# Kernel optimization log

Hardware: AMD Instinct MI355X
Metric: run time of the kernel (lower is better)

Reference implementation:

```python
import jax, jax.numpy as jnp
import numpy as np

NODE_DIM = 128
CAT = 16
N_NODES = 100000
N_EDGES = 200000
N_SCALARS = 6
INPUT_DIM = 5 * NODE_DIM + 5 * CAT + N_SCALARS  # 726
CELL_H, NET_H, OUT = 192, 128, 128
EPS = 1e-5


def setup_inputs() -> dict:
    key = jax.random.key(0)
    ks = jax.random.split(key, 24)
    inp = {
        'h_nodes': jax.random.normal(ks[0], (N_NODES, NODE_DIM), jnp.float32),
        'edge_scalars': jax.random.normal(ks[1], (N_EDGES, N_SCALARS), jnp.float32),
        'edge_src': jax.random.randint(ks[2], (N_EDGES,), 0, N_NODES),
        'edge_dst': jax.random.randint(ks[3], (N_EDGES,), 0, N_NODES),
        'edge_type': jax.random.randint(ks[4], (N_EDGES,), 0, 2),
        'cell_type_src': jax.random.randint(ks[5], (N_EDGES,), 0, 256),
        'cell_type_dst': jax.random.randint(ks[6], (N_EDGES,), 0, 256),
        'pin_role_src': jax.random.randint(ks[7], (N_EDGES,), 0, 64),
        'pin_role_dst': jax.random.randint(ks[8], (N_EDGES,), 0, 64),
        # embedding tables
        'emb_edge_type': jax.random.normal(ks[9], (2, CAT), jnp.float32),
        'emb_cell_type': jax.random.normal(ks[10], (256, CAT), jnp.float32),
        'emb_pin_role': jax.random.normal(ks[11], (64, CAT), jnp.float32),
        # cell MLP params
        'cell_W1': jax.random.normal(ks[12], (INPUT_DIM, CELL_H), jnp.float32) * (1.0 / np.sqrt(INPUT_DIM)),
        'cell_b1': jnp.zeros((CELL_H,), jnp.float32),
        'cell_g': jnp.ones((CELL_H,), jnp.float32),
        'cell_beta': jnp.zeros((CELL_H,), jnp.float32),
        'cell_W2': jax.random.normal(ks[13], (CELL_H, OUT), jnp.float32) * (1.0 / np.sqrt(CELL_H)),
        'cell_b2': jnp.zeros((OUT,), jnp.float32),
        # net MLP params
        'net_W1': jax.random.normal(ks[14], (INPUT_DIM, NET_H), jnp.float32) * (1.0 / np.sqrt(INPUT_DIM)),
        'net_b1': jnp.zeros((NET_H,), jnp.float32),
        'net_g': jnp.ones((NET_H,), jnp.float32),
        'net_beta': jnp.zeros((NET_H,), jnp.float32),
        'net_W2': jax.random.normal(ks[15], (NET_H, OUT), jnp.float32) * (1.0 / np.sqrt(NET_H)),
        'net_b2': jnp.zeros((OUT,), jnp.float32),
    }
    return inp


def _oov(x, n):
    return jnp.where((x >= 0) & (x < n), x, 0)


def _mlp(x, W1, b1, g, beta, W2, b2):
    h = x @ W1 + b1
    mu = jnp.mean(h, axis=-1, keepdims=True)
    var = jnp.mean(jnp.square(h - mu), axis=-1, keepdims=True)
    h = (h - mu) * jax.lax.rsqrt(var + EPS) * g + beta
    h = jax.nn.relu(h)
    return h @ W2 + b2


def reference(h_nodes, edge_scalars, emb_edge_type, emb_cell_type, emb_pin_role,
              cell_W1, cell_b1, cell_g, cell_beta, cell_W2, cell_b2,
              net_W1, net_b1, net_g, net_beta, net_W2, net_b2,
              edge_src, edge_dst, edge_type, cell_type_src, cell_type_dst,
              pin_role_src, pin_role_dst):
    h_u = h_nodes[edge_src]                      # [E, D]
    h_v = h_nodes[edge_dst]
    h_prod = h_u * h_v
    h_abs_diff = jnp.abs(h_u - h_v)
    h_signed_diff = h_v - h_u
    e_et = emb_edge_type[_oov(edge_type, emb_edge_type.shape[0])]
    e_ct_s = emb_cell_type[_oov(cell_type_src, emb_cell_type.shape[0])]
    e_ct_d = emb_cell_type[_oov(cell_type_dst, emb_cell_type.shape[0])]
    e_pr_s = emb_pin_role[_oov(pin_role_src, emb_pin_role.shape[0])]
    e_pr_d = emb_pin_role[_oov(pin_role_dst, emb_pin_role.shape[0])]
    scal = jnp.clip(edge_scalars, -10.0, 10.0)
    feat = jnp.concatenate([h_u, h_v, h_prod, h_abs_diff, h_signed_diff,
                            e_et, e_ct_s, e_ct_d, e_pr_s, e_pr_d, scal], axis=-1)  # [E, 726]
    out_cell = _mlp(feat, cell_W1, cell_b1, cell_g, cell_beta, cell_W2, cell_b2)
    out_net = _mlp(feat, net_W1, net_b1, net_g, net_beta, net_W2, net_b2)
    et = edge_type[:, None]
    h_edges = jnp.where(et == 0, out_cell, jnp.where(et == 1, out_net, jnp.zeros_like(out_cell)))
    return h_edges
```

## Files before the change

kernel.cpp:

```cpp
#include <hip/hip_runtime.h>

#define KS   23
#define BM   32
#define CHK  136

typedef short bfrag8 __attribute__((ext_vector_type(8)));
typedef float f32x4 __attribute__((ext_vector_type(4)));

__device__ __forceinline__ unsigned short f2bf(float f) {
  union { float f; unsigned u; } v; v.f = f;
  unsigned r = v.u + 0x7fffu + ((v.u >> 16) & 1u);
  return (unsigned short)(r >> 16);
}
__device__ __forceinline__ unsigned pk2(float a, float b) {
  return (unsigned)f2bf(a) | ((unsigned)f2bf(b) << 16);
}

__global__ void prep_weights(const float* __restrict__ cW1, const float* __restrict__ nW1,
                             const float* __restrict__ cW2, const float* __restrict__ nW2,
                             unsigned short* __restrict__ w1c, unsigned short* __restrict__ w1n,
                             unsigned short* __restrict__ w2c, unsigned short* __restrict__ w2n,
                             int* __restrict__ cnt) {
  int i = blockIdx.x * blockDim.x + threadIdx.x;
  if (i == 0) { cnt[0] = 0; cnt[1] = 0; }
  const int T0 = 12 * KS * 512, T1 = 8 * KS * 512, T2 = 8 * 6 * 512, T3 = 8 * 4 * 512;
  const int tot = T0 + T1 + T2 + T3;
  for (; i < tot; i += gridDim.x * blockDim.x) {
    int idx = i;
    const float* src; unsigned short* dst; int N, Kreal, KSm, rel;
    if (idx < T0)              { src = cW1; dst = w1c; N = 192; Kreal = 726; KSm = KS; rel = idx; }
    else if ((idx -= T0) < T1) { src = nW1; dst = w1n; N = 128; Kreal = 726; KSm = KS; rel = idx; }
    else if ((idx -= T1) < T2) { src = cW2; dst = w2c; N = 128; Kreal = 192; KSm = 6;  rel = idx; }
    else { idx -= T2;            src = nW2; dst = w2n; N = 128; Kreal = 128; KSm = 4;  rel = idx; }
    int blk = rel >> 9, within = rel & 511;
    int l = within >> 3, e = within & 7;
    int n16 = blk / KSm, k32 = blk - n16 * KSm;
    int n = n16 * 16 + (l & 15);
    int k = k32 * 32 + ((l >> 4) * 8) + e;
    dst[rel] = f2bf(k < Kreal ? src[(size_t)k * N + n] : 0.f);
  }
}

__global__ void compact_edges(const int* __restrict__ et,
                              const int* __restrict__ esrc, const int* __restrict__ edst,
                              const int* __restrict__ cts, const int* __restrict__ ctd,
                              const int* __restrict__ prs, const int* __restrict__ prd,
                              int* __restrict__ cnt, int4* __restrict__ r0, int4* __restrict__ r1,
                              float* __restrict__ out, int n) {
  int i = blockIdx.x * blockDim.x + threadIdx.x;
  for (; i < n; i += gridDim.x * blockDim.x) {
    int ty = et[i];
    if (ty == 0 || ty == 1) {
      int c1 = cts[i]; c1 = ((unsigned)c1 < 256u) ? c1 : 0;
      int c2 = ctd[i]; c2 = ((unsigned)c2 < 256u) ? c2 : 0;
      int p1 = prs[i]; p1 = ((unsigned)p1 < 64u)  ? p1 : 0;
      int p2 = prd[i]; p2 = ((unsigned)p2 < 64u)  ? p2 : 0;
      int4 rec; rec.x = esrc[i]; rec.y = edst[i]; rec.z = i;
      rec.w = c1 | (c2 << 8) | (p1 << 16) | (p2 << 22);
      if (ty == 0) r0[atomicAdd(&cnt[0], 1)] = rec;
      else         r1[atomicAdd(&cnt[1], 1)] = rec;
    } else {
      float4 z = make_float4(0.f, 0.f, 0.f, 0.f);
      float4* po = (float4*)(out + (size_t)i * 128);
      #pragma unroll
      for (int j = 0; j < 32; ++j) po[j] = z;
    }
  }
}

template <int CH>
__device__ __forceinline__ void mlp_tile(
    char* smraw, int* sEid, int tile, int c, int etv,
    const int4* __restrict__ rec,
    const float* __restrict__ h_nodes, const float* __restrict__ edge_scalars,
    const float* __restrict__ emb_et, const float* __restrict__ emb_ct, const float* __restrict__ emb_pr,
    const unsigned short* __restrict__ w1f, const unsigned short* __restrict__ w2f,
    const float* __restrict__ b1, const float* __restrict__ g,
    const float* __restrict__ beta, const float* __restrict__ b2,
    float* __restrict__ out)
{
  constexpr int NF  = CH / 64;
  constexpr int KS2 = CH / 32;
  constexpr int CHP = CH + 8;
  unsigned short (*ch)[BM][CHK] = (unsigned short (*)[BM][CHK])smraw;
  unsigned short (*hb)[CHP]     = (unsigned short (*)[CHP])(smraw + 17408);
  float (*red)[BM][2] = (float (*)[BM][2])(smraw + 17408 + 12800);
  float (*murs)[2]    = (float (*)[2])(smraw + 17408 + 12800 + 1024);

  const int t    = threadIdx.x;
  const int lane = t & 63;
  const int wid  = t >> 6;
  const int lrow = lane & 15;
  const int kq   = (lane >> 4) * 8;
  const int base = tile * BM;
  const int r    = t >> 3;
  const int l8   = t & 7;

  float b1r[NF], gr[NF], ber[NF];
  #pragma unroll
  for (int nf = 0; nf < NF; ++nf) {
    int n = wid * (CH / 4) + nf * 16 + lrow;
    b1r[nf] = b1[n]; gr[nf] = g[n]; ber[nf] = beta[n];
  }
  float b2r[2];
  #pragma unroll
  for (int nf2 = 0; nf2 < 2; ++nf2) b2r[nf2] = b2[wid * 32 + nf2 * 16 + lrow];

  const int idx  = base + r;
  const bool valid = idx < c;
  int4 q = rec[valid ? idx : (c - 1)];
  if (l8 == 0) sEid[r] = valid ? q.z : -1;

  const float* bu = h_nodes + (size_t)q.x * 128;
  const float* bv = h_nodes + (size_t)q.y * 128;
  float4 ub[4], vb[4];
  #pragma unroll
  for (int j = 0; j < 4; ++j) {
    const int d = (l8 + 8 * j) * 4;
    ub[j] = *(const float4*)(bu + d);
    vb[j] = *(const float4*)(bv + d);
  }
  const int pk = q.w;
  const int c1 = pk & 255, c2 = (pk >> 8) & 255, p1 = (pk >> 16) & 63, p2 = (pk >> 22) & 63;
  const float* tp = (l8 == 0) ? emb_et + etv * 16
                  : (l8 == 1) ? emb_ct + c1 * 16
                  : (l8 == 2) ? emb_ct + c2 * 16
                  : (l8 == 3) ? emb_pr + p1 * 16
                  :             emb_pr + p2 * 16;
  float4 e4[4];
  if (l8 < 5) {
    #pragma unroll
    for (int j = 0; j < 4; ++j) e4[j] = ((const float4*)tp)[j];
  }
  float2 sc2[3];
  if (l8 == 5) {
    const float2* sp = (const float2*)(edge_scalars + (size_t)q.z * 6);
    #pragma unroll
    for (int j = 0; j < 3; ++j) sc2[j] = sp[j];
  }

  auto writeChunk = [&](int cc) {
    unsigned short (*buf)[CHK] = ch[cc & 1];
    if (cc < 5) {
      #pragma unroll
      for (int j = 0; j < 4; ++j) {
        const int d = (l8 + 8 * j) * 4;
        float ua[4] = {ub[j].x, ub[j].y, ub[j].z, ub[j].w};
        float va[4] = {vb[j].x, vb[j].y, vb[j].z, vb[j].w};
        float x[4];
        #pragma unroll
        for (int e = 0; e < 4; ++e) {
          x[e] = (cc == 0) ? ua[e]
               : (cc == 1) ? va[e]
               : (cc == 2) ? ua[e] * va[e]
               : (cc == 3) ? fabsf(ua[e] - va[e])
               :             va[e] - ua[e];
        }
        *(uint2*)&buf[r][d] = make_uint2(pk2(x[0], x[1]), pk2(x[2], x[3]));
      }
    } else {
      if (l8 < 5) {
        float va[16];
        #pragma unroll
        for (int j = 0; j < 4; ++j) {
          va[4 * j + 0] = e4[j].x; va[4 * j + 1] = e4[j].y;
          va[4 * j + 2] = e4[j].z; va[4 * j + 3] = e4[j].w;
        }
        uint4 w0 = make_uint4(pk2(va[0], va[1]), pk2(va[2], va[3]), pk2(va[4], va[5]), pk2(va[6], va[7]));
        uint4 w1_ = make_uint4(pk2(va[8], va[9]), pk2(va[10], va[11]), pk2(va[12], va[13]), pk2(va[14], va[15]));
        *(uint4*)&buf[r][l8 * 16 + 0] = w0;
        *(uint4*)&buf[r][l8 * 16 + 8] = w1_;
      } else if (l8 == 5) {
        float sv[6] = {sc2[0].x, sc2[0].y, sc2[1].x, sc2[1].y, sc2[2].x, sc2[2].y};
        #pragma unroll
        for (int j = 0; j < 6; ++j) sv[j] = fminf(fmaxf(sv[j], -10.f), 10.f);
        uint4 w0 = make_uint4(pk2(sv[0], sv[1]), pk2(sv[2], sv[3]), pk2(sv[4], sv[5]), 0u);
        *(uint4*)&buf[r][80] = w0;
        *(uint4*)&buf[r][88] = make_uint4(0u, 0u, 0u, 0u);
      }
    }
  };

  f32x4 acc1[2][NF];
  #pragma unroll
  for (int mf = 0; mf < 2; ++mf)
    #pragma unroll
    for (int nf = 0; nf < NF; ++nf) acc1[mf][nf] = 0;
  const unsigned short* wb = w1f + ((size_t)wid * NF * KS) * 512 + (size_t)lane * 8;

  writeChunk(0);
  __syncthreads();
  #pragma unroll
  for (int cc = 0; cc < 6; ++cc) {
    if (cc < 5) writeChunk(cc + 1);
    const int ks = (cc < 5) ? 4 : 3;
    unsigned short (*buf)[CHK] = ch[cc & 1];
    #pragma unroll
    for (int k = 0; k < 4; ++k) {
      if (k >= ks) break;
      const int kk = cc * 4 + k;
      bfrag8 a0 = *(const bfrag8*)&buf[lrow][k * 32 + kq];
      bfrag8 a1 = *(const bfrag8*)&buf[16 + lrow][k * 32 + kq];
      #pragma unroll
      for (int nf = 0; nf < NF; ++nf) {
        bfrag8 bf = *(const bfrag8*)(wb + ((size_t)nf * KS + kk) * 512);
        acc1[0][nf] = __builtin_amdgcn_mfma_f32_16x16x32_bf16(a0, bf, acc1[0][nf], 0, 0, 0);
        acc1[1][nf] = __builtin_amdgcn_mfma_f32_16x16x32_bf16(a1, bf, acc1[1][nf], 0, 0, 0);
      }
    }
    __syncthreads();
  }

  bfrag8 cr[KS2][2];
  const unsigned short* wb2 = w2f + (size_t)lane * 8;
  #pragma unroll
  for (int k2 = 0; k2 < KS2; ++k2)
    #pragma unroll
    for (int nf2 = 0; nf2 < 2; ++nf2)
      cr[k2][nf2] = *(const bfrag8*)(wb2 + ((size_t)(2 * wid + nf2) * KS2 + k2) * 512);

  float sums[2][4], sqs[2][4];
  #pragma unroll
  for (int mf = 0; mf < 2; ++mf)
    #pragma unroll
    for (int rg = 0; rg < 4; ++rg) {
      float s = 0.f, qd = 0.f;
      #pragma unroll
      for (int nf = 0; nf < NF; ++nf) {
        float v = acc1[mf][nf][rg] + b1r[nf];
        acc1[mf][nf][rg] = v;
        s += v; qd += v * v;
      }
      sums[mf][rg] = s; sqs[mf][rg] = qd;
    }
  #pragma unroll
  for (int d = 1; d < 16; d <<= 1) {
    #pragma unroll
    for (int mf = 0; mf < 2; ++mf)
      #pragma unroll
      for (int rg = 0; rg < 4; ++rg) {
        sums[mf][rg] += __shfl_xor(sums[mf][rg], d);
        sqs[mf][rg]  += __shfl_xor(sqs[mf][rg], d);
      }
  }
  if (lrow == 0) {
    const int qr = lane >> 4;
    #pragma unroll
    for (int mf = 0; mf < 2; ++mf)
      #pragma unroll
      for (int rg = 0; rg < 4; ++rg) {
        int row = mf * 16 + qr * 4 + rg;
        red[wid][row][0] = sums[mf][rg];
        red[wid][row][1] = sqs[mf][rg];
      }
  }
  __syncthreads();
  if (t < BM) {
    float ss = red[0][t][0] + red[1][t][0] + red[2][t][0] + red[3][t][0];
    float qq = red[0][t][1] + red[1][t][1] + red[2][t][1] + red[3][t][1];
    float m = ss * (1.f / CH);
    float va = fmaxf(qq * (1.f / CH) - m * m, 0.f);
    murs[t][0] = m;
    murs[t][1] = rsqrtf(va + 1e-5f);
  }
  __syncthreads();

  #pragma unroll
  for (int mf = 0; mf < 2; ++mf)
    #pragma unroll
    for (int rg = 0; rg < 4; ++rg) {
      int row = mf * 16 + (lane >> 4) * 4 + rg;
      float m = murs[row][0], rv = murs[row][1];
      #pragma unroll
      for (int nf = 0; nf < NF; ++nf) {
        float v = (acc1[mf][nf][rg] - m) * rv * gr[nf] + ber[nf];
        hb[row][wid * (CH / 4) + nf * 16 + lrow] = f2bf(fmaxf(v, 0.f));
      }
    }
  __syncthreads();

  f32x4 acc2[2][2];
  #pragma unroll
  for (int mf = 0; mf < 2; ++mf) { acc2[mf][0] = 0; acc2[mf][1] = 0; }
  #pragma unroll
  for (int k2 = 0; k2 < KS2; ++k2) {
    bfrag8 a0 = *(const bfrag8*)&hb[lrow][k2 * 32 + kq];
    bfrag8 a1 = *(const bfrag8*)&hb[16 + lrow][k2 * 32 + kq];
    #pragma unroll
    for (int nf2 = 0; nf2 < 2; ++nf2) {
      acc2[0][nf2] = __builtin_amdgcn_mfma_f32_16x16x32_bf16(a0, cr[k2][nf2], acc2[0][nf2], 0, 0, 0);
      acc2[1][nf2] = __builtin_amdgcn_mfma_f32_16x16x32_bf16(a1, cr[k2][nf2], acc2[1][nf2], 0, 0, 0);
    }
  }

  #pragma unroll
  for (int mf = 0; mf < 2; ++mf)
    #pragma unroll
    for (int rg = 0; rg < 4; ++rg) {
      int row = mf * 16 + (lane >> 4) * 4 + rg;
      int eid = sEid[row];
      if (eid >= 0) {
        float* po = out + (size_t)eid * 128 + wid * 32 + lrow;
        #pragma unroll
        for (int nf2 = 0; nf2 < 2; ++nf2)
          po[nf2 * 16] = acc2[mf][nf2][rg] + b2r[nf2];
      }
    }
}

struct Args {
  const float *h_nodes, *edge_scalars;
  const float *emb_et, *emb_ct, *emb_pr;
  const unsigned short *w1c, *w2c;
  const float *cb1, *cg, *cbe, *cb2;
  const unsigned short *w1n, *w2n;
  const float *nb1, *ng, *nbe, *nb2;
  const int *cnt;
  const int4 *r0, *r1;
  float* out;
};

__global__ __launch_bounds__(256, 4) void edge_mlp_all(Args A) {
  __shared__ alignas(16) char smraw[17408 + 12800 + 1024 + 256];
  __shared__ int sEid[BM];
  const int c0 = A.cnt[0];
  const int nb0 = (c0 + BM - 1) / BM;
  const int b = blockIdx.x;
  if (b < nb0) {
    mlp_tile<192>(smraw, sEid, b, c0, 0, A.r0, A.h_nodes, A.edge_scalars,
                  A.emb_et, A.emb_ct, A.emb_pr, A.w1c, A.w2c,
                  A.cb1, A.cg, A.cbe, A.cb2, A.out);
  } else {
    const int c1 = A.cnt[1];
    const int t2 = b - nb0;
    if (t2 * BM < c1)
      mlp_tile<128>(smraw, sEid, t2, c1, 1, A.r1, A.h_nodes, A.edge_scalars,
                    A.emb_et, A.emb_ct, A.emb_pr, A.w1n, A.w2n,
                    A.nb1, A.ng, A.nbe, A.nb2, A.out);
  }
}

extern "C" void kernel_launch(void* const* d_in, const int* in_sizes, int n_in,
                              void* d_out, int out_size, void* d_ws, size_t ws_size,
                              hipStream_t stream) {
  (void)n_in; (void)out_size; (void)ws_size;
  const float* h_nodes      = (const float*)d_in[0];
  const float* edge_scalars = (const float*)d_in[1];
  const int*   edge_src     = (const int*)d_in[2];
  const int*   edge_dst     = (const int*)d_in[3];
  const int*   edge_type    = (const int*)d_in[4];
  const int*   ct_s         = (const int*)d_in[5];
  const int*   ct_d         = (const int*)d_in[6];
  const int*   pr_s         = (const int*)d_in[7];
  const int*   pr_d         = (const int*)d_in[8];
  const float* emb_et       = (const float*)d_in[9];
  const float* emb_ct       = (const float*)d_in[10];
  const float* emb_pr       = (const float*)d_in[11];
  const float* cW1 = (const float*)d_in[12];
  const float* cb1 = (const float*)d_in[13];
  const float* cg  = (const float*)d_in[14];
  const float* cbe = (const float*)d_in[15];
  const float* cW2 = (const float*)d_in[16];
  const float* cb2 = (const float*)d_in[17];
  const float* nW1 = (const float*)d_in[18];
  const float* nb1 = (const float*)d_in[19];
  const float* ng  = (const float*)d_in[20];
  const float* nbe = (const float*)d_in[21];
  const float* nW2 = (const float*)d_in[22];
  const float* nb2 = (const float*)d_in[23];
  const int n_edges = in_sizes[2];
  float* out = (float*)d_out;

  char* ws = (char*)d_ws;
  int* cnt = (int*)ws;
  int4* r0 = (int4*)(ws + 256);
  int4* r1 = r0 + n_edges;
  size_t woff = (256 + (size_t)2 * n_edges * sizeof(int4) + 255) & ~(size_t)255;
  unsigned short* w1c = (unsigned short*)(ws + woff);
  unsigned short* w1n = w1c + 12 * KS * 512;
  unsigned short* w2c = w1n + 8 * KS * 512;
  unsigned short* w2n = w2c + 8 * 6 * 512;

  prep_weights<<<1080, 256, 0, stream>>>(cW1, nW1, cW2, nW2, w1c, w1n, w2c, w2n, cnt);
  compact_edges<<<(n_edges + 255) / 256, 256, 0, stream>>>(edge_type, edge_src, edge_dst,
                                                           ct_s, ct_d, pr_s, pr_d,
                                                           cnt, r0, r1, out, n_edges);

  Args A;
  A.h_nodes = h_nodes; A.edge_scalars = edge_scalars;
  A.emb_et = emb_et; A.emb_ct = emb_ct; A.emb_pr = emb_pr;
  A.w1c = w1c; A.w2c = w2c; A.cb1 = cb1; A.cg = cg; A.cbe = cbe; A.cb2 = cb2;
  A.w1n = w1n; A.w2n = w2n; A.nb1 = nb1; A.ng = ng; A.nbe = nbe; A.nb2 = nb2;
  A.cnt = cnt; A.r0 = r0; A.r1 = r1; A.out = out;

  const int nbAll = (n_edges + BM - 1) / BM + 2;
  edge_mlp_all<<<nbAll, 256, 0, stream>>>(A);
}
```

Measured before the change: 224.6 us.

## Double edge tile to 64 rows with 512 threads and alias hidden buffer

Raises the edge tile from 32 to 64 rows and the block from 256 to 512 threads, arranged as a 2x4 wave grid (row half by column quarter). Each W1/W2 weight fragment loaded from global memory now serves twice as many edges. The embedding and scalar chunk is written first and used for the first MFMA pass, so the derived node-feature chunks are produced one step ahead. The hidden-activation buffer now overlaps the chunk staging area to keep LDS usage bounded. The cost is fewer resident blocks per CU, since the 512-thread blocks need more registers and LDS, plus a larger wasted tail tile.

```diff
diff --git a/kernel.cpp b/kernel.cpp
--- a/kernel.cpp
+++ b/kernel.cpp
@@ -1,7 +1,7 @@
 #include <hip/hip_runtime.h>
 
 #define KS   23
-#define BM   32
+#define BM   64
 #define CHK  136
 
 typedef short bfrag8 __attribute__((ext_vector_type(8)));
@@ -83,13 +83,15 @@
   constexpr int KS2 = CH / 32;
   constexpr int CHP = CH + 8;
   unsigned short (*ch)[BM][CHK] = (unsigned short (*)[BM][CHK])smraw;
-  unsigned short (*hb)[CHP]     = (unsigned short (*)[CHP])(smraw + 17408);
-  float (*red)[BM][2] = (float (*)[BM][2])(smraw + 17408 + 12800);
-  float (*murs)[2]    = (float (*)[2])(smraw + 17408 + 12800 + 1024);
+  unsigned short (*hb)[CHP]     = (unsigned short (*)[CHP])smraw;
+  float (*red)[BM][2] = (float (*)[BM][2])(smraw + 34816);
+  float (*murs)[2]    = (float (*)[2])(smraw + 34816 + 2048);
 
   const int t    = threadIdx.x;
   const int lane = t & 63;
   const int wid  = t >> 6;
+  const int mi   = wid & 1;
+  const int ni   = wid >> 1;
   const int lrow = lane & 15;
   const int kq   = (lane >> 4) * 8;
   const int base = tile * BM;
@@ -99,12 +101,12 @@
   float b1r[NF], gr[NF], ber[NF];
   #pragma unroll
   for (int nf = 0; nf < NF; ++nf) {
-    int n = wid * (CH / 4) + nf * 16 + lrow;
+    int n = ni * (CH / 4) + nf * 16 + lrow;
     b1r[nf] = b1[n]; gr[nf] = g[n]; ber[nf] = beta[n];
   }
   float b2r[2];
   #pragma unroll
-  for (int nf2 = 0; nf2 < 2; ++nf2) b2r[nf2] = b2[wid * 32 + nf2 * 16 + lrow];
+  for (int nf2 = 0; nf2 < 2; ++nf2) b2r[nf2] = b2[ni * 32 + nf2 * 16 + lrow];
 
   const int idx  = base + r;
   const bool valid = idx < c;
@@ -120,64 +122,58 @@
     ub[j] = *(const float4*)(bu + d);
     vb[j] = *(const float4*)(bv + d);
   }
-  const int pk = q.w;
-  const int c1 = pk & 255, c2 = (pk >> 8) & 255, p1 = (pk >> 16) & 63, p2 = (pk >> 22) & 63;
-  const float* tp = (l8 == 0) ? emb_et + etv * 16
-                  : (l8 == 1) ? emb_ct + c1 * 16
-                  : (l8 == 2) ? emb_ct + c2 * 16
-                  : (l8 == 3) ? emb_pr + p1 * 16
-                  :             emb_pr + p2 * 16;
-  float4 e4[4];
-  if (l8 < 5) {
-    #pragma unroll
-    for (int j = 0; j < 4; ++j) e4[j] = ((const float4*)tp)[j];
-  }
-  float2 sc2[3];
-  if (l8 == 5) {
-    const float2* sp = (const float2*)(edge_scalars + (size_t)q.z * 6);
-    #pragma unroll
-    for (int j = 0; j < 3; ++j) sc2[j] = sp[j];
-  }
-
-  auto writeChunk = [&](int cc) {
-    unsigned short (*buf)[CHK] = ch[cc & 1];
-    if (cc < 5) {
+  {
+    const int pk = q.w;
+    const int c1 = pk & 255, c2 = (pk >> 8) & 255, p1 = (pk >> 16) & 63, p2 = (pk >> 22) & 63;
+    if (l8 < 5) {
+      const float* tp = (l8 == 0) ? emb_et + etv * 16
+                      : (l8 == 1) ? emb_ct + c1 * 16
+                      : (l8 == 2) ? emb_ct + c2 * 16
+                      : (l8 == 3) ? emb_pr + p1 * 16
+                      :             emb_pr + p2 * 16;
+      float4 e4[4];
+      #pragma unroll
+      for (int j = 0; j < 4; ++j) e4[j] = ((const float4*)tp)[j];
+      float va[16];
       #pragma unroll
       for (int j = 0; j < 4; ++j) {
-        const int d = (l8 + 8 * j) * 4;
-        float ua[4] = {ub[j].x, ub[j].y, ub[j].z, ub[j].w};
-        float va[4] = {vb[j].x, vb[j].y, vb[j].z, vb[j].w};
-        float x[4];
-        #pragma unroll
-        for (int e = 0; e < 4; ++e) {
-          x[e] = (cc == 0) ? ua[e]
-               : (cc == 1) ? va[e]
-               : (cc == 2) ? ua[e] * va[e]
-               : (cc == 3) ? fabsf(ua[e] - va[e])
-               :             va[e] - ua[e];
-        }
-        *(uint2*)&buf[r][d] = make_uint2(pk2(x[0], x[1]), pk2(x[2], x[3]));
-      }
-    } else {
-      if (l8 < 5) {
-        float va[16];
-        #pragma unroll
-        for (int j = 0; j < 4; ++j) {
-          va[4 * j + 0] = e4[j].x; va[4 * j + 1] = e4[j].y;
-          va[4 * j + 2] = e4[j].z; va[4 * j + 3] = e4[j].w;
-        }
-        uint4 w0 = make_uint4(pk2(va[0], va[1]), pk2(va[2], va[3]), pk2(va[4], va[5]), pk2(va[6], va[7]));
-        uint4 w1_ = make_uint4(pk2(va[8], va[9]), pk2(va[10], va[11]), pk2(va[12], va[13]), pk2(va[14], va[15]));
-        *(uint4*)&buf[r][l8 * 16 + 0] = w0;
-        *(uint4*)&buf[r][l8 * 16 + 8] = w1_;
-      } else if (l8 == 5) {
-        float sv[6] = {sc2[0].x, sc2[0].y, sc2[1].x, sc2[1].y, sc2[2].x, sc2[2].y};
-        #pragma unroll
-        for (int j = 0; j < 6; ++j) sv[j] = fminf(fmaxf(sv[j], -10.f), 10.f);
-        uint4 w0 = make_uint4(pk2(sv[0], sv[1]), pk2(sv[2], sv[3]), pk2(sv[4], sv[5]), 0u);
-        *(uint4*)&buf[r][80] = w0;
-        *(uint4*)&buf[r][88] = make_uint4(0u, 0u, 0u, 0u);
-      }
+        va[4 * j + 0] = e4[j].x; va[4 * j + 1] = e4[j].y;
+        va[4 * j + 2] = e4[j].z; va[4 * j + 3] = e4[j].w;
+      }
+      *(uint4*)&ch[0][r][l8 * 16 + 0] =
+        make_uint4(pk2(va[0], va[1]), pk2(va[2], va[3]), pk2(va[4], va[5]), pk2(va[6], va[7]));
+      *(uint4*)&ch[0][r][l8 * 16 + 8] =
+        make_uint4(pk2(va[8], va[9]), pk2(va[10], va[11]), pk2(va[12], va[13]), pk2(va[14], va[15]));
+    } else if (l8 == 5) {
+      const float2* sp = (const float2*)(edge_scalars + (size_t)q.z * 6);
+      float2 sc2[3];
+      #pragma unroll
+      for (int j = 0; j < 3; ++j) sc2[j] = sp[j];
+      float sv[6] = {sc2[0].x, sc2[0].y, sc2[1].x, sc2[1].y, sc2[2].x, sc2[2].y};
+      #pragma unroll
+      for (int j = 0; j < 6; ++j) sv[j] = fminf(fmaxf(sv[j], -10.f), 10.f);
+      *(uint4*)&ch[0][r][80] = make_uint4(pk2(sv[0], sv[1]), pk2(sv[2], sv[3]), pk2(sv[4], sv[5]), 0u);
+      *(uint4*)&ch[0][r][88] = make_uint4(0u, 0u, 0u, 0u);
+    }
+  }
+
+  auto writeDerived = [&](int seg) {
+    unsigned short (*buf)[CHK] = ch[(seg + 1) & 1];
+    #pragma unroll
+    for (int j = 0; j < 4; ++j) {
+      const int d = (l8 + 8 * j) * 4;
+      float ua[4] = {ub[j].x, ub[j].y, ub[j].z, ub[j].w};
+      float va[4] = {vb[j].x, vb[j].y, vb[j].z, vb[j].w};
+      float x[4];
+      #pragma unroll
+      for (int e = 0; e < 4; ++e) {
+        x[e] = (seg == 0) ? ua[e]
+             : (seg == 1) ? va[e]
+             : (seg == 2) ? ua[e] * va[e]
+             : (seg == 3) ? fabsf(ua[e] - va[e])
+             :              va[e] - ua[e];
+      }
+      *(uint2*)&buf[r][d] = make_uint2(pk2(x[0], x[1]), pk2(x[2], x[3]));
     }
   };
 
@@ -186,21 +182,21 @@
   for (int mf = 0; mf < 2; ++mf)
     #pragma unroll
     for (int nf = 0; nf < NF; ++nf) acc1[mf][nf] = 0;
-  const unsigned short* wb = w1f + ((size_t)wid * NF * KS) * 512 + (size_t)lane * 8;
-
-  writeChunk(0);
+  const unsigned short* wb = w1f + ((size_t)ni * NF * KS) * 512 + (size_t)lane * 8;
+
   __syncthreads();
   #pragma unroll
   for (int cc = 0; cc < 6; ++cc) {
-    if (cc < 5) writeChunk(cc + 1);
-    const int ks = (cc < 5) ? 4 : 3;
+    if (cc < 5) writeDerived(cc);
+    const int kb = (cc == 0) ? 20 : (cc - 1) * 4;
+    const int ks = (cc == 0) ? 3 : 4;
     unsigned short (*buf)[CHK] = ch[cc & 1];
     #pragma unroll
     for (int k = 0; k < 4; ++k) {
       if (k >= ks) break;
-      const int kk = cc * 4 + k;
-      bfrag8 a0 = *(const bfrag8*)&buf[lrow][k * 32 + kq];
-      bfrag8 a1 = *(const bfrag8*)&buf[16 + lrow][k * 32 + kq];
+      const int kk = kb + k;
+      bfrag8 a0 = *(const bfrag8*)&buf[32 * mi + lrow][k * 32 + kq];
+      bfrag8 a1 = *(const bfrag8*)&buf[32 * mi + 16 + lrow][k * 32 + kq];
       #pragma unroll
       for (int nf = 0; nf < NF; ++nf) {
         bfrag8 bf = *(const bfrag8*)(wb + ((size_t)nf * KS + kk) * 512);
@@ -217,7 +213,7 @@
   for (int k2 = 0; k2 < KS2; ++k2)
     #pragma unroll
     for (int nf2 = 0; nf2 < 2; ++nf2)
-      cr[k2][nf2] = *(const bfrag8*)(wb2 + ((size_t)(2 * wid + nf2) * KS2 + k2) * 512);
+      cr[k2][nf2] = *(const bfrag8*)(wb2 + ((size_t)(ni * 2 + nf2) * KS2 + k2) * 512);
 
   float sums[2][4], sqs[2][4];
   #pragma unroll
@@ -249,9 +245,9 @@
     for (int mf = 0; mf < 2; ++mf)
       #pragma unroll
       for (int rg = 0; rg < 4; ++rg) {
-        int row = mf * 16 + qr * 4 + rg;
-        red[wid][row][0] = sums[mf][rg];
-        red[wid][row][1] = sqs[mf][rg];
+        int row = 32 * mi + 16 * mf + qr * 4 + rg;
+        red[ni][row][0] = sums[mf][rg];
+        red[ni][row][1] = sqs[mf][rg];
       }
   }
   __syncthreads();
@@ -269,12 +265,12 @@
   for (int mf = 0; mf < 2; ++mf)
     #pragma unroll
     for (int rg = 0; rg < 4; ++rg) {
-      int row = mf * 16 + (lane >> 4) * 4 + rg;
+      int row = 32 * mi + 16 * mf + (lane >> 4) * 4 + rg;
       float m = murs[row][0], rv = murs[row][1];
       #pragma unroll
       for (int nf = 0; nf < NF; ++nf) {
         float v = (acc1[mf][nf][rg] - m) * rv * gr[nf] + ber[nf];
-        hb[row][wid * (CH / 4) + nf * 16 + lrow] = f2bf(fmaxf(v, 0.f));
+        hb[row][ni * (CH / 4) + nf * 16 + lrow] = f2bf(fmaxf(v, 0.f));
       }
     }
   __syncthreads();
@@ -284,8 +280,8 @@
   for (int mf = 0; mf < 2; ++mf) { acc2[mf][0] = 0; acc2[mf][1] = 0; }
   #pragma unroll
   for (int k2 = 0; k2 < KS2; ++k2) {
-    bfrag8 a0 = *(const bfrag8*)&hb[lrow][k2 * 32 + kq];
-    bfrag8 a1 = *(const bfrag8*)&hb[16 + lrow][k2 * 32 + kq];
+    bfrag8 a0 = *(const bfrag8*)&hb[32 * mi + lrow][k2 * 32 + kq];
+    bfrag8 a1 = *(const bfrag8*)&hb[32 * mi + 16 + lrow][k2 * 32 + kq];
     #pragma unroll
     for (int nf2 = 0; nf2 < 2; ++nf2) {
       acc2[0][nf2] = __builtin_amdgcn_mfma_f32_16x16x32_bf16(a0, cr[k2][nf2], acc2[0][nf2], 0, 0, 0);
@@ -297,10 +293,10 @@
   for (int mf = 0; mf < 2; ++mf)
     #pragma unroll
     for (int rg = 0; rg < 4; ++rg) {
-      int row = mf * 16 + (lane >> 4) * 4 + rg;
+      int row = 32 * mi + 16 * mf + (lane >> 4) * 4 + rg;
       int eid = sEid[row];
       if (eid >= 0) {
-        float* po = out + (size_t)eid * 128 + wid * 32 + lrow;
+        float* po = out + (size_t)eid * 128 + ni * 32 + lrow;
         #pragma unroll
         for (int nf2 = 0; nf2 < 2; ++nf2)
           po[nf2 * 16] = acc2[mf][nf2][rg] + b2r[nf2];
@@ -320,8 +316,8 @@
   float* out;
 };
 
-__global__ __launch_bounds__(256, 4) void edge_mlp_all(Args A) {
-  __shared__ alignas(16) char smraw[17408 + 12800 + 1024 + 256];
+__global__ __launch_bounds__(512, 4) void edge_mlp_all(Args A) {
+  __shared__ alignas(16) char smraw[34816 + 2048 + 512];
   __shared__ int sEid[BM];
   const int c0 = A.cnt[0];
   const int nb0 = (c0 + BM - 1) / BM;
@@ -394,5 +390,5 @@
   A.cnt = cnt; A.r0 = r0; A.r1 = r1; A.out = out;
 
   const int nbAll = (n_edges + BM - 1) / BM + 2;
-  edge_mlp_all<<<nbAll, 256, 0, stream>>>(A);
-}
+  edge_mlp_all<<<nbAll, 512, 0, stream>>>(A);
+}
```

Measured after the change: 231.4 us. +3.1%, slower.

## Give each wave its own 32-edge tile and drop block-level syncs

Applied to the files above, without the earlier changes.

Restructures the edge MLP so each wavefront processes a full 32-edge tile across all output columns, instead of four waves splitting the N dimension of one tile. The gathered node rows are converted to bf16 straight into MFMA A-fragments in registers, and the product and difference features are computed per fragment, which removes the shared-memory feature staging and all __syncthreads. LayerNorm reductions stay within the wave through shuffles, and the embedding and scalar features go through a small per-wave LDS region. In exchange each wave now reads the full W1/W2 weight fragments from global/L2, with four times as many weight loads per tile. It also holds many more accumulator registers, and launch bounds drop to 2 blocks per CU. Differences are now computed from bf16-rounded inputs, which slightly changes numerics.

```diff
diff --git a/kernel.cpp b/kernel.cpp
--- a/kernel.cpp
+++ b/kernel.cpp
@@ -1,8 +1,6 @@
 #include <hip/hip_runtime.h>
 
-#define KS   23
-#define BM   32
-#define CHK  136
+#define KS 23
 
 typedef short bfrag8 __attribute__((ext_vector_type(8)));
 typedef float f32x4 __attribute__((ext_vector_type(4)));
@@ -14,6 +12,11 @@
 }
 __device__ __forceinline__ unsigned pk2(float a, float b) {
   return (unsigned)f2bf(a) | ((unsigned)f2bf(b) << 16);
+}
+__device__ __forceinline__ float bf2f(short s) {
+  union { unsigned u; float f; } v;
+  v.u = ((unsigned)(unsigned short)s) << 16;
+  return v.f;
 }
 
 __global__ void prep_weights(const float* __restrict__ cW1, const float* __restrict__ nW1,
@@ -68,9 +71,35 @@
   }
 }
 
+__device__ __forceinline__ void loadrow(const float* __restrict__ p, int kq, bfrag8 f[4]) {
+  #pragma unroll
+  for (int j = 0; j < 4; ++j) {
+    float4 x = *(const float4*)(p + j * 32 + kq);
+    float4 y = *(const float4*)(p + j * 32 + kq + 4);
+    union { bfrag8 b; uint4 q; } r;
+    r.q = make_uint4(pk2(x.x, x.y), pk2(x.z, x.w), pk2(y.x, y.y), pk2(y.z, y.w));
+    f[j] = r.b;
+  }
+}
+
+__device__ __forceinline__ bfrag8 dfrag(bfrag8 u, bfrag8 v, int op) {
+  unsigned w[4];
+  #pragma unroll
+  for (int i = 0; i < 4; ++i) {
+    float u0 = bf2f(u[2 * i]),     v0 = bf2f(v[2 * i]);
+    float u1 = bf2f(u[2 * i + 1]), v1 = bf2f(v[2 * i + 1]);
+    float x0 = (op == 0) ? u0 * v0 : (op == 1) ? fabsf(u0 - v0) : v0 - u0;
+    float x1 = (op == 0) ? u1 * v1 : (op == 1) ? fabsf(u1 - v1) : v1 - u1;
+    w[i] = pk2(x0, x1);
+  }
+  union { bfrag8 b; uint4 q; } r;
+  r.q = make_uint4(w[0], w[1], w[2], w[3]);
+  return r.b;
+}
+
 template <int CH>
-__device__ __forceinline__ void mlp_tile(
-    char* smraw, int* sEid, int tile, int c, int etv,
+__device__ __forceinline__ void mlp_wave(
+    char* wls, int lane, int tile, int c, int etv,
     const int4* __restrict__ rec,
     const float* __restrict__ h_nodes, const float* __restrict__ edge_scalars,
     const float* __restrict__ emb_et, const float* __restrict__ emb_ct, const float* __restrict__ emb_pr,
@@ -79,145 +108,109 @@
     const float* __restrict__ beta, const float* __restrict__ b2,
     float* __restrict__ out)
 {
-  constexpr int NF  = CH / 64;
+  constexpr int NF  = CH / 16;
   constexpr int KS2 = CH / 32;
-  constexpr int CHP = CH + 8;
-  unsigned short (*ch)[BM][CHK] = (unsigned short (*)[BM][CHK])smraw;
-  unsigned short (*hb)[CHP]     = (unsigned short (*)[CHP])(smraw + 17408);
-  float (*red)[BM][2] = (float (*)[BM][2])(smraw + 17408 + 12800);
-  float (*murs)[2]    = (float (*)[2])(smraw + 17408 + 12800 + 1024);
-
-  const int t    = threadIdx.x;
-  const int lane = t & 63;
-  const int wid  = t >> 6;
+  constexpr int HST = CH + 8;
+  constexpr int EST = 104;
+  unsigned short (*hb)[HST]  = (unsigned short (*)[HST])wls;
+  unsigned short (*emb)[EST] = (unsigned short (*)[EST])wls;
+
   const int lrow = lane & 15;
-  const int kq   = (lane >> 4) * 8;
-  const int base = tile * BM;
-  const int r    = t >> 3;
-  const int l8   = t & 7;
-
-  float b1r[NF], gr[NF], ber[NF];
-  #pragma unroll
-  for (int nf = 0; nf < NF; ++nf) {
-    int n = wid * (CH / 4) + nf * 16 + lrow;
-    b1r[nf] = b1[n]; gr[nf] = g[n]; ber[nf] = beta[n];
-  }
-  float b2r[2];
-  #pragma unroll
-  for (int nf2 = 0; nf2 < 2; ++nf2) b2r[nf2] = b2[wid * 32 + nf2 * 16 + lrow];
-
-  const int idx  = base + r;
-  const bool valid = idx < c;
-  int4 q = rec[valid ? idx : (c - 1)];
-  if (l8 == 0) sEid[r] = valid ? q.z : -1;
-
-  const float* bu = h_nodes + (size_t)q.x * 128;
-  const float* bv = h_nodes + (size_t)q.y * 128;
-  float4 ub[4], vb[4];
-  #pragma unroll
-  for (int j = 0; j < 4; ++j) {
-    const int d = (l8 + 8 * j) * 4;
-    ub[j] = *(const float4*)(bu + d);
-    vb[j] = *(const float4*)(bv + d);
-  }
-  const int pk = q.w;
-  const int c1 = pk & 255, c2 = (pk >> 8) & 255, p1 = (pk >> 16) & 63, p2 = (pk >> 22) & 63;
-  const float* tp = (l8 == 0) ? emb_et + etv * 16
-                  : (l8 == 1) ? emb_ct + c1 * 16
-                  : (l8 == 2) ? emb_ct + c2 * 16
-                  : (l8 == 3) ? emb_pr + p1 * 16
-                  :             emb_pr + p2 * 16;
-  float4 e4[4];
-  if (l8 < 5) {
-    #pragma unroll
-    for (int j = 0; j < 4; ++j) e4[j] = ((const float4*)tp)[j];
-  }
-  float2 sc2[3];
-  if (l8 == 5) {
-    const float2* sp = (const float2*)(edge_scalars + (size_t)q.z * 6);
-    #pragma unroll
-    for (int j = 0; j < 3; ++j) sc2[j] = sp[j];
-  }
-
-  auto writeChunk = [&](int cc) {
-    unsigned short (*buf)[CHK] = ch[cc & 1];
-    if (cc < 5) {
-      #pragma unroll
-      for (int j = 0; j < 4; ++j) {
-        const int d = (l8 + 8 * j) * 4;
-        float ua[4] = {ub[j].x, ub[j].y, ub[j].z, ub[j].w};
-        float va[4] = {vb[j].x, vb[j].y, vb[j].z, vb[j].w};
-        float x[4];
-        #pragma unroll
-        for (int e = 0; e < 4; ++e) {
-          x[e] = (cc == 0) ? ua[e]
-               : (cc == 1) ? va[e]
-               : (cc == 2) ? ua[e] * va[e]
-               : (cc == 3) ? fabsf(ua[e] - va[e])
-               :             va[e] - ua[e];
-        }
-        *(uint2*)&buf[r][d] = make_uint2(pk2(x[0], x[1]), pk2(x[2], x[3]));
+  const int grp  = lane >> 4;
+  const int kq   = grp * 8;
+  const int base = tile * 32;
+
+  int4 qa = rec[min(base + lrow, c - 1)];
+  int4 qb = rec[min(base + 16 + lrow, c - 1)];
+
+  {
+    const int rr = lane >> 1, hf = lane & 1;
+    int4 qe = rec[min(base + rr, c - 1)];
+    const int pk = qe.w;
+    if (hf == 0) {
+      const float* tps[3] = { emb_et + etv * 16,
+                              emb_ct + (pk & 255) * 16,
+                              emb_ct + ((pk >> 8) & 255) * 16 };
+      #pragma unroll
+      for (int tb = 0; tb < 3; ++tb) {
+        const float4* tp = (const float4*)tps[tb];
+        float4 a = tp[0], b4 = tp[1], c4 = tp[2], d4 = tp[3];
+        *(uint4*)&emb[rr][tb * 16 + 0] =
+          make_uint4(pk2(a.x, a.y), pk2(a.z, a.w), pk2(b4.x, b4.y), pk2(b4.z, b4.w));
+        *(uint4*)&emb[rr][tb * 16 + 8] =
+          make_uint4(pk2(c4.x, c4.y), pk2(c4.z, c4.w), pk2(d4.x, d4.y), pk2(d4.z, d4.w));
       }
     } else {
-      if (l8 < 5) {
-        float va[16];
-        #pragma unroll
-        for (int j = 0; j < 4; ++j) {
-          va[4 * j + 0] = e4[j].x; va[4 * j + 1] = e4[j].y;
-          va[4 * j + 2] = e4[j].z; va[4 * j + 3] = e4[j].w;
-        }
-        uint4 w0 = make_uint4(pk2(va[0], va[1]), pk2(va[2], va[3]), pk2(va[4], va[5]), pk2(va[6], va[7]));
-        uint4 w1_ = make_uint4(pk2(va[8], va[9]), pk2(va[10], va[11]), pk2(va[12], va[13]), pk2(va[14], va[15]));
-        *(uint4*)&buf[r][l8 * 16 + 0] = w0;
-        *(uint4*)&buf[r][l8 * 16 + 8] = w1_;
-      } else if (l8 == 5) {
-        float sv[6] = {sc2[0].x, sc2[0].y, sc2[1].x, sc2[1].y, sc2[2].x, sc2[2].y};
-        #pragma unroll
-        for (int j = 0; j < 6; ++j) sv[j] = fminf(fmaxf(sv[j], -10.f), 10.f);
-        uint4 w0 = make_uint4(pk2(sv[0], sv[1]), pk2(sv[2], sv[3]), pk2(sv[4], sv[5]), 0u);
-        *(uint4*)&buf[r][80] = w0;
-        *(uint4*)&buf[r][88] = make_uint4(0u, 0u, 0u, 0u);
-      }
-    }
-  };
+      const float* tps[2] = { emb_pr + ((pk >> 16) & 63) * 16,
+                              emb_pr + ((pk >> 22) & 63) * 16 };
+      #pragma unroll
+      for (int tb = 0; tb < 2; ++tb) {
+        const float4* tp = (const float4*)tps[tb];
+        float4 a = tp[0], b4 = tp[1], c4 = tp[2], d4 = tp[3];
+        *(uint4*)&emb[rr][48 + tb * 16 + 0] =
+          make_uint4(pk2(a.x, a.y), pk2(a.z, a.w), pk2(b4.x, b4.y), pk2(b4.z, b4.w));
+        *(uint4*)&emb[rr][48 + tb * 16 + 8] =
+          make_uint4(pk2(c4.x, c4.y), pk2(c4.z, c4.w), pk2(d4.x, d4.y), pk2(d4.z, d4.w));
+      }
+      const float2* sp = (const float2*)(edge_scalars + (size_t)qe.z * 6);
+      float2 s0 = sp[0], s1 = sp[1], s2 = sp[2];
+      float v0 = fminf(fmaxf(s0.x, -10.f), 10.f), v1 = fminf(fmaxf(s0.y, -10.f), 10.f);
+      float v2 = fminf(fmaxf(s1.x, -10.f), 10.f), v3 = fminf(fmaxf(s1.y, -10.f), 10.f);
+      float v4 = fminf(fmaxf(s2.x, -10.f), 10.f), v5 = fminf(fmaxf(s2.y, -10.f), 10.f);
+      *(uint4*)&emb[rr][80] = make_uint4(pk2(v0, v1), pk2(v2, v3), pk2(v4, v5), 0u);
+      *(uint4*)&emb[rr][88] = make_uint4(0u, 0u, 0u, 0u);
+    }
+  }
+
+  bfrag8 ua[4], va[4], ub[4], vb[4];
+  loadrow(h_nodes + (size_t)qa.x * 128, kq, ua);
+  loadrow(h_nodes + (size_t)qa.y * 128, kq, va);
+  loadrow(h_nodes + (size_t)qb.x * 128, kq, ub);
+  loadrow(h_nodes + (size_t)qb.y * 128, kq, vb);
 
   f32x4 acc1[2][NF];
   #pragma unroll
   for (int mf = 0; mf < 2; ++mf)
     #pragma unroll
     for (int nf = 0; nf < NF; ++nf) acc1[mf][nf] = 0;
-  const unsigned short* wb = w1f + ((size_t)wid * NF * KS) * 512 + (size_t)lane * 8;
-
-  writeChunk(0);
-  __syncthreads();
-  #pragma unroll
-  for (int cc = 0; cc < 6; ++cc) {
-    if (cc < 5) writeChunk(cc + 1);
-    const int ks = (cc < 5) ? 4 : 3;
-    unsigned short (*buf)[CHK] = ch[cc & 1];
+  const unsigned short* wbl = w1f + (size_t)lane * 8;
+
+  #pragma unroll
+  for (int seg = 0; seg < 5; ++seg) {
     #pragma unroll
     for (int k = 0; k < 4; ++k) {
-      if (k >= ks) break;
-      const int kk = cc * 4 + k;
-      bfrag8 a0 = *(const bfrag8*)&buf[lrow][k * 32 + kq];
-      bfrag8 a1 = *(const bfrag8*)&buf[16 + lrow][k * 32 + kq];
+      const int kk = seg * 4 + k;
+      bfrag8 a0, a1;
+      if (seg == 0)      { a0 = ua[k]; a1 = ub[k]; }
+      else if (seg == 1) { a0 = va[k]; a1 = vb[k]; }
+      else { a0 = dfrag(ua[k], va[k], seg - 2); a1 = dfrag(ub[k], vb[k], seg - 2); }
       #pragma unroll
       for (int nf = 0; nf < NF; ++nf) {
-        bfrag8 bf = *(const bfrag8*)(wb + ((size_t)nf * KS + kk) * 512);
+        bfrag8 bf = *(const bfrag8*)(wbl + ((size_t)(nf * KS + kk)) * 512);
         acc1[0][nf] = __builtin_amdgcn_mfma_f32_16x16x32_bf16(a0, bf, acc1[0][nf], 0, 0, 0);
         acc1[1][nf] = __builtin_amdgcn_mfma_f32_16x16x32_bf16(a1, bf, acc1[1][nf], 0, 0, 0);
       }
     }
-    __syncthreads();
-  }
-
-  bfrag8 cr[KS2][2];
-  const unsigned short* wb2 = w2f + (size_t)lane * 8;
-  #pragma unroll
-  for (int k2 = 0; k2 < KS2; ++k2)
-    #pragma unroll
-    for (int nf2 = 0; nf2 < 2; ++nf2)
-      cr[k2][nf2] = *(const bfrag8*)(wb2 + ((size_t)(2 * wid + nf2) * KS2 + k2) * 512);
+  }
+  #pragma unroll
+  for (int k = 0; k < 3; ++k) {
+    const int kk = 20 + k;
+    bfrag8 a0 = *(const bfrag8*)&emb[lrow][k * 32 + kq];
+    bfrag8 a1 = *(const bfrag8*)&emb[16 + lrow][k * 32 + kq];
+    #pragma unroll
+    for (int nf = 0; nf < NF; ++nf) {
+      bfrag8 bf = *(const bfrag8*)(wbl + ((size_t)(nf * KS + kk)) * 512);
+      acc1[0][nf] = __builtin_amdgcn_mfma_f32_16x16x32_bf16(a0, bf, acc1[0][nf], 0, 0, 0);
+      acc1[1][nf] = __builtin_amdgcn_mfma_f32_16x16x32_bf16(a1, bf, acc1[1][nf], 0, 0, 0);
+    }
+  }
+
+  float b1r[NF], gr[NF], ber[NF];
+  #pragma unroll
+  for (int nf = 0; nf < NF; ++nf) {
+    int n = nf * 16 + lrow;
+    b1r[nf] = b1[n]; gr[nf] = g[n]; ber[nf] = beta[n];
+  }
 
   float sums[2][4], sqs[2][4];
   #pragma unroll
@@ -243,53 +236,40 @@
         sqs[mf][rg]  += __shfl_xor(sqs[mf][rg], d);
       }
   }
-  if (lrow == 0) {
-    const int qr = lane >> 4;
-    #pragma unroll
-    for (int mf = 0; mf < 2; ++mf)
-      #pragma unroll
-      for (int rg = 0; rg < 4; ++rg) {
-        int row = mf * 16 + qr * 4 + rg;
-        red[wid][row][0] = sums[mf][rg];
-        red[wid][row][1] = sqs[mf][rg];
-      }
-  }
-  __syncthreads();
-  if (t < BM) {
-    float ss = red[0][t][0] + red[1][t][0] + red[2][t][0] + red[3][t][0];
-    float qq = red[0][t][1] + red[1][t][1] + red[2][t][1] + red[3][t][1];
-    float m = ss * (1.f / CH);
-    float va = fmaxf(qq * (1.f / CH) - m * m, 0.f);
-    murs[t][0] = m;
-    murs[t][1] = rsqrtf(va + 1e-5f);
-  }
-  __syncthreads();
-
   #pragma unroll
   for (int mf = 0; mf < 2; ++mf)
     #pragma unroll
     for (int rg = 0; rg < 4; ++rg) {
-      int row = mf * 16 + (lane >> 4) * 4 + rg;
-      float m = murs[row][0], rv = murs[row][1];
+      float mu = sums[mf][rg] * (1.f / CH);
+      float var = fmaxf(sqs[mf][rg] * (1.f / CH) - mu * mu, 0.f);
+      float rs = rsqrtf(var + 1e-5f);
+      int row = mf * 16 + grp * 4 + rg;
       #pragma unroll
       for (int nf = 0; nf < NF; ++nf) {
-        float v = (acc1[mf][nf][rg] - m) * rv * gr[nf] + ber[nf];
-        hb[row][wid * (CH / 4) + nf * 16 + lrow] = f2bf(fmaxf(v, 0.f));
-      }
-    }
-  __syncthreads();
-
-  f32x4 acc2[2][2];
-  #pragma unroll
-  for (int mf = 0; mf < 2; ++mf) { acc2[mf][0] = 0; acc2[mf][1] = 0; }
+        float v = (acc1[mf][nf][rg] - mu) * rs * gr[nf] + ber[nf];
+        hb[row][nf * 16 + lrow] = f2bf(fmaxf(v, 0.f));
+      }
+    }
+
+  float b2r[8];
+  #pragma unroll
+  for (int nf2 = 0; nf2 < 8; ++nf2) b2r[nf2] = b2[nf2 * 16 + lrow];
+
+  f32x4 acc2[2][8];
+  #pragma unroll
+  for (int mf = 0; mf < 2; ++mf)
+    #pragma unroll
+    for (int nf2 = 0; nf2 < 8; ++nf2) acc2[mf][nf2] = 0;
+  const unsigned short* wbl2 = w2f + (size_t)lane * 8;
   #pragma unroll
   for (int k2 = 0; k2 < KS2; ++k2) {
     bfrag8 a0 = *(const bfrag8*)&hb[lrow][k2 * 32 + kq];
     bfrag8 a1 = *(const bfrag8*)&hb[16 + lrow][k2 * 32 + kq];
     #pragma unroll
-    for (int nf2 = 0; nf2 < 2; ++nf2) {
-      acc2[0][nf2] = __builtin_amdgcn_mfma_f32_16x16x32_bf16(a0, cr[k2][nf2], acc2[0][nf2], 0, 0, 0);
-      acc2[1][nf2] = __builtin_amdgcn_mfma_f32_16x16x32_bf16(a1, cr[k2][nf2], acc2[1][nf2], 0, 0, 0);
+    for (int nf2 = 0; nf2 < 8; ++nf2) {
+      bfrag8 bf = *(const bfrag8*)(wbl2 + ((size_t)(nf2 * KS2 + k2)) * 512);
+      acc2[0][nf2] = __builtin_amdgcn_mfma_f32_16x16x32_bf16(a0, bf, acc2[0][nf2], 0, 0, 0);
+      acc2[1][nf2] = __builtin_amdgcn_mfma_f32_16x16x32_bf16(a1, bf, acc2[1][nf2], 0, 0, 0);
     }
   }
 
@@ -297,12 +277,12 @@
   for (int mf = 0; mf < 2; ++mf)
     #pragma unroll
     for (int rg = 0; rg < 4; ++rg) {
-      int row = mf * 16 + (lane >> 4) * 4 + rg;
-      int eid = sEid[row];
-      if (eid >= 0) {
-        float* po = out + (size_t)eid * 128 + wid * 32 + lrow;
+      const int rowLow = grp * 4 + rg;
+      const int eid = __shfl(mf ? qb.z : qa.z, rowLow);
+      if (base + mf * 16 + rowLow < c) {
+        float* po = out + (size_t)eid * 128 + lrow;
         #pragma unroll
-        for (int nf2 = 0; nf2 < 2; ++nf2)
+        for (int nf2 = 0; nf2 < 8; ++nf2)
           po[nf2 * 16] = acc2[mf][nf2][rg] + b2r[nf2];
       }
     }
@@ -320,21 +300,23 @@
   float* out;
 };
 
-__global__ __launch_bounds__(256, 4) void edge_mlp_all(Args A) {
-  __shared__ alignas(16) char smraw[17408 + 12800 + 1024 + 256];
-  __shared__ int sEid[BM];
+__global__ __launch_bounds__(256, 2) void edge_mlp_all(Args A) {
+  __shared__ alignas(16) char smraw[4 * 12800];
+  const int wid = threadIdx.x >> 6;
+  const int lane = threadIdx.x & 63;
+  char* wls = smraw + wid * 12800;
+  const int w = blockIdx.x * 4 + wid;
   const int c0 = A.cnt[0];
-  const int nb0 = (c0 + BM - 1) / BM;
-  const int b = blockIdx.x;
-  if (b < nb0) {
-    mlp_tile<192>(smraw, sEid, b, c0, 0, A.r0, A.h_nodes, A.edge_scalars,
+  const int t0 = (c0 + 31) >> 5;
+  if (w < t0) {
+    mlp_wave<192>(wls, lane, w, c0, 0, A.r0, A.h_nodes, A.edge_scalars,
                   A.emb_et, A.emb_ct, A.emb_pr, A.w1c, A.w2c,
                   A.cb1, A.cg, A.cbe, A.cb2, A.out);
   } else {
     const int c1 = A.cnt[1];
-    const int t2 = b - nb0;
-    if (t2 * BM < c1)
-      mlp_tile<128>(smraw, sEid, t2, c1, 1, A.r1, A.h_nodes, A.edge_scalars,
+    const int w1 = w - t0;
+    if (w1 * 32 < c1)
+      mlp_wave<128>(wls, lane, w1, c1, 1, A.r1, A.h_nodes, A.edge_scalars,
                     A.emb_et, A.emb_ct, A.emb_pr, A.w1n, A.w2n,
                     A.nb1, A.ng, A.nbe, A.nb2, A.out);
   }
@@ -393,6 +375,7 @@
   A.w1n = w1n; A.w2n = w2n; A.nb1 = nb1; A.ng = ng; A.nbe = nbe; A.nb2 = nb2;
   A.cnt = cnt; A.r0 = r0; A.r1 = r1; A.out = out;
 
-  const int nbAll = (n_edges + BM - 1) / BM + 2;
+  const int waves = (n_edges + 31) / 32 + 2;
+  const int nbAll = (waves + 3) / 4;
   edge_mlp_all<<<nbAll, 256, 0, stream>>>(A);
 }
```

Measured after the change: 298.5 us. 1.33x slower.
